# Kernel optimization log

Hardware: AMD Instinct MI355X
Metric: run time of the kernel (lower is better)

The kernel has to match this reference:

```python
import jax, jax.numpy as jnp
import numpy as np

N_NODES = 100000
N_EDGES = 1600000
IN_DIM = 256
OUT_DIM = 128


def setup_inputs() -> dict:
    key = jax.random.key(0)
    k1, k2, k3, k4 = jax.random.split(key, 4)
    x = jax.random.normal(k1, (N_NODES, IN_DIM), dtype=jnp.float32)
    edge_list = jax.random.randint(k2, (2, N_EDGES), 0, N_NODES, dtype=jnp.int64)
    # xavier_uniform with gain=1.414
    gW = 1.414 * np.sqrt(6.0 / (IN_DIM + OUT_DIM))
    W = jax.random.uniform(k3, (IN_DIM, OUT_DIM), dtype=jnp.float32, minval=-gW, maxval=gW)
    ga = 1.414 * np.sqrt(6.0 / (2 * OUT_DIM + 1))
    a = jax.random.uniform(k4, (2 * OUT_DIM, 1), dtype=jnp.float32, minval=-ga, maxval=ga)
    return {"x": x, "edge_list": edge_list, "W": W, "a": a}


def reference(x, edge_list, W, a):
    N = x.shape[0]
    src, dst = edge_list[0], edge_list[1]
    h = x @ W  # [N, out_dim]
    # cat([h[src], h[dst]]) @ a  ==  h[src] @ a[:d] + h[dst] @ a[d:]
    d = h.shape[1]
    s_src = (h @ a[:d]).ravel()  # [N]
    s_dst = (h @ a[d:]).ravel()  # [N]
    e = jax.nn.leaky_relu(s_src[src] + s_dst[dst], negative_slope=0.2)  # [E]
    # sparse softmax over rows (segments = src node)
    seg_max = jax.ops.segment_max(e, src, num_segments=N)  # [N]
    ex = jnp.exp(e - seg_max[src])  # [E]
    denom = jax.ops.segment_sum(ex, src, num_segments=N)  # [N]
    attn = ex / jnp.where(denom > 0, denom, 1.0)[src]  # [E]
    # sparse aggregate: h_prime[i] = sum_{edges (i,j)} attn_ij * h[j]
    h_prime = jax.ops.segment_sum(attn[:, None] * h[dst], src, num_segments=N)  # [N, d]
    return jax.nn.elu(h_prime)
```

## Files before the change

### kernel.cpp

```cpp
#include <hip/hip_runtime.h>
#include <hip/hip_bf16.h>
#include <cstdint>
#include <cstddef>

#define NN 100000
#define NE 1600000
#define KD 256
#define OD 128
#define NB 391
#define CAP 8192
#define NGB 782

typedef __attribute__((ext_vector_type(8))) __bf16 bf16x8;
typedef __attribute__((ext_vector_type(4))) float f32x4;
typedef __attribute__((ext_vector_type(8))) unsigned short ushort8;

static __device__ __forceinline__ unsigned short f2bf(float f) {
  return __builtin_bit_cast(unsigned short, (__bf16)f);
}
static __device__ __forceinline__ float bflo(unsigned p) {
  return __builtin_bit_cast(float, p << 16);
}
static __device__ __forceinline__ float bfhi(unsigned p) {
  return __builtin_bit_cast(float, p & 0xffff0000u);
}

__global__ void prep_wt_k(const float* __restrict__ W, unsigned short* __restrict__ Wt,
                          int* __restrict__ bcur) {
  const int i = blockIdx.x * 256 + threadIdx.x;
  const int k = i >> 7;
  const int n = i & 127;
  Wt[n * KD + k] = f2bf(W[i]);
  if (i < NB) bcur[i] = i * CAP;
}

__global__ __launch_bounds__(512, 4) void fused_k(
    const float* __restrict__ x, const unsigned short* __restrict__ Wt,
    const float* __restrict__ a, unsigned short* __restrict__ h,
    float* __restrict__ ssrc, float* __restrict__ sdst,
    const int* __restrict__ el, int* __restrict__ bcur,
    unsigned* __restrict__ stage) {
  __shared__ alignas(16) char smem[65536];
  const int t = threadIdx.x;

  if (blockIdx.x < NGB) {
    unsigned short* Bl = (unsigned short*)smem;
#pragma unroll
    for (int it = 0; it < 8; ++it) {
      const int c = it * 512 + t;
      const int r = c >> 5;
      const int c16 = c & 31;
      const ushort8 v = *(const ushort8*)(Wt + r * 256 + c16 * 8);
      const int byt = (r * 512 + c16 * 16) ^ ((r & 7) << 4);
      *(ushort8*)((char*)Bl + byt) = v;
    }
    const int lane = t & 63;
    const int wave = t >> 6;
    const int col = lane & 15;
    const int kg = lane >> 4;
    const int m0 = blockIdx.x * 128 + wave * 16;
    const int arow = m0 + col;
    const bool rowok = arow < NN;
    const float* __restrict__ xrow = x + (size_t)arow * KD;
    __syncthreads();

    f32x4 acc[8];
#pragma unroll
    for (int i = 0; i < 8; ++i) acc[i] = (f32x4)0.0f;

#pragma unroll
    for (int s = 0; s < 8; ++s) {
      const int kk = s * 32 + kg * 8;
      bf16x8 af = (bf16x8)(__bf16)0.0f;
      if (rowok) {
        const float4 f0 = *(const float4*)(xrow + kk);
        const float4 f1 = *(const float4*)(xrow + kk + 4);
        af[0] = (__bf16)f0.x; af[1] = (__bf16)f0.y; af[2] = (__bf16)f0.z; af[3] = (__bf16)f0.w;
        af[4] = (__bf16)f1.x; af[5] = (__bf16)f1.y; af[6] = (__bf16)f1.z; af[7] = (__bf16)f1.w;
      }
#pragma unroll
      for (int nt = 0; nt < 8; ++nt) {
        const int n = nt * 16 + col;
        const int byt = (n * 512 + s * 64 + kg * 16) ^ ((col & 7) << 4);
        const ushort8 bu = *(const ushort8*)((const char*)Bl + byt);
        const bf16x8 bf = __builtin_bit_cast(bf16x8, bu);
        acc[nt] = __builtin_amdgcn_mfma_f32_16x16x32_bf16(af, bf, acc[nt], 0, 0, 0);
      }
    }

    float ps[4] = {0.f, 0.f, 0.f, 0.f};
    float pd[4] = {0.f, 0.f, 0.f, 0.f};
#pragma unroll
    for (int nt = 0; nt < 8; ++nt) {
      const int n = nt * 16 + col;
      const float av = a[n];
      const float av2 = a[OD + n];
#pragma unroll
      for (int r = 0; r < 4; ++r) {
        const float v = acc[nt][r];
        const int row = m0 + kg * 4 + r;
        if (row < NN) h[(size_t)row * OD + n] = f2bf(v);
        ps[r] += v * av;
        pd[r] += v * av2;
      }
    }
#pragma unroll
    for (int off = 1; off < 16; off <<= 1) {
#pragma unroll
      for (int r = 0; r < 4; ++r) {
        ps[r] += __shfl_xor(ps[r], off, 64);
        pd[r] += __shfl_xor(pd[r], off, 64);
      }
    }
    if (col == 0) {
#pragma unroll
      for (int r = 0; r < 4; ++r) {
        const int row = m0 + kg * 4 + r;
        if (row < NN) {
          ssrc[row] = ps[r] * 1.442695041f;
          sdst[row] = pd[r] * 1.442695041f;
        }
      }
    }
  } else {
    unsigned* sorted = (unsigned*)smem;
    unsigned short* bkid = (unsigned short*)(smem + 16384);
    int* hist  = (int*)(smem + 24576);
    int* off   = (int*)(smem + 26144);
    int* cur   = (int*)(smem + 27712);
    int* delta = (int*)(smem + 29276);
    const int te = (blockIdx.x - NGB) * 4096 + t * 8;
    int s[8], d[8];
    bool valid[8];
#pragma unroll
    for (int u = 0; u < 8; ++u) valid[u] = (te + u) < NE;
    if (te + 7 < NE) {
      const int4 a0 = *(const int4*)(el + te);
      const int4 a1 = *(const int4*)(el + te + 4);
      const int4 b0 = *(const int4*)(el + NE + te);
      const int4 b1 = *(const int4*)(el + NE + te + 4);
      s[0] = a0.x; s[1] = a0.y; s[2] = a0.z; s[3] = a0.w;
      s[4] = a1.x; s[5] = a1.y; s[6] = a1.z; s[7] = a1.w;
      d[0] = b0.x; d[1] = b0.y; d[2] = b0.z; d[3] = b0.w;
      d[4] = b1.x; d[5] = b1.y; d[6] = b1.z; d[7] = b1.w;
    } else {
#pragma unroll
      for (int u = 0; u < 8; ++u) {
        s[u] = valid[u] ? el[te + u] : 0;
        d[u] = valid[u] ? el[NE + te + u] : 0;
      }
    }
    for (int i = t; i <= NB; i += 512) hist[i] = 0;
    __syncthreads();
#pragma unroll
    for (int u = 0; u < 8; ++u)
      if (valid[u]) atomicAdd(&hist[s[u] >> 8], 1);
    __syncthreads();
    if (t < 64) {
      int v[7];
      int sum = 0;
#pragma unroll
      for (int i = 0; i < 7; ++i) {
        const int idx = t * 7 + i;
        v[i] = (idx <= NB) ? hist[idx] : 0;
        sum += v[i];
      }
      int pre = sum;
#pragma unroll
      for (int o = 1; o < 64; o <<= 1) {
        const int nb = __shfl_up(pre, o, 64);
        if (t >= o) pre += nb;
      }
      pre -= sum;
      int run = pre;
#pragma unroll
      for (int i = 0; i < 7; ++i) {
        const int idx = t * 7 + i;
        if (idx <= NB) off[idx] = run;
        run += v[i];
      }
    }
    __syncthreads();
    for (int i = t; i < NB; i += 512) cur[i] = off[i];
    __syncthreads();
#pragma unroll
    for (int u = 0; u < 8; ++u)
      if (valid[u]) {
        const int b = s[u] >> 8;
        const int p = atomicAdd(&cur[b], 1);
        sorted[p] = ((unsigned)(s[u] & 255) << 17) | (unsigned)d[u];
        bkid[p] = (unsigned short)b;
      }
    __syncthreads();
    for (int b = t; b < NB; b += 512) {
      const int len = off[b + 1] - off[b];
      if (len > 0) {
        const int gb = atomicAdd(&bcur[b], len);
        delta[b] = gb - off[b];
      }
    }
    __syncthreads();
    const int n = off[NB];
    for (int i = t; i < n; i += 512) {
      const int b = bkid[i];
      const int pos = delta[b] + i;
      if (pos < (b + 1) * CAP) stage[pos] = sorted[i];
    }
  }
}

__global__ __launch_bounds__(512) void bscan_k(const int* __restrict__ bcur,
                                               int* __restrict__ bbase) {
  __shared__ int tmp[512];
  const int t = threadIdx.x;
  int v = 0;
  if (t < NB) {
    v = bcur[t] - t * CAP;
    v = v > CAP ? CAP : v;
  }
  tmp[t] = v;
  __syncthreads();
  for (int o = 1; o < 512; o <<= 1) {
    const int add = (t >= o) ? tmp[t - o] : 0;
    __syncthreads();
    tmp[t] += add;
    __syncthreads();
  }
  if (t < NB) bbase[t] = tmp[t] - v;
}

__global__ __launch_bounds__(256) void place2_k(const unsigned* __restrict__ stage,
                                                const int* __restrict__ bcur,
                                                const int* __restrict__ bbase,
                                                int* __restrict__ csrd,
                                                int* __restrict__ cnt,
                                                int* __restrict__ rowstart) {
  __shared__ unsigned ebuf[CAP];
  __shared__ int hist2[256];
  __shared__ int exc[256];
  __shared__ int cur2[256];
  const int b = blockIdx.x;
  const int t = threadIdx.x;
  int tot = bcur[b] - b * CAP;
  tot = tot > CAP ? CAP : tot;
  const int base = bbase[b];
  hist2[t] = 0;
  for (int i = t; i < tot; i += 256) ebuf[i] = stage[(size_t)b * CAP + i];
  __syncthreads();
  for (int i = t; i < tot; i += 256) atomicAdd(&hist2[ebuf[i] >> 17], 1);
  __syncthreads();
  if (t < 64) {
    int v[4];
    int sum = 0;
#pragma unroll
    for (int i = 0; i < 4; ++i) { v[i] = hist2[t * 4 + i]; sum += v[i]; }
    int pre = sum;
#pragma unroll
    for (int o = 1; o < 64; o <<= 1) {
      const int nb = __shfl_up(pre, o, 64);
      if (t >= o) pre += nb;
    }
    pre -= sum;
    int run = pre;
#pragma unroll
    for (int i = 0; i < 4; ++i) { exc[t * 4 + i] = run; run += v[i]; }
  }
  __syncthreads();
  const int node = b * 256 + t;
  if (node < NN) {
    cnt[node] = hist2[t];
    rowstart[node] = base + exc[t];
  }
  cur2[t] = exc[t];
  __syncthreads();
  for (int i = t; i < tot; i += 256) {
    const unsigned u = ebuf[i];
    const int p = atomicAdd(&cur2[u >> 17], 1);
    csrd[base + p] = (int)(u & 0x1ffffu);
  }
}

__global__ __launch_bounds__(256) void aggr_k(
    const unsigned short* __restrict__ h, const int* __restrict__ csrd,
    const int* __restrict__ rowstart, const int* __restrict__ cnt,
    const float* __restrict__ ssrc, const float* __restrict__ sdst,
    float* __restrict__ out) {
  const int lane = threadIdx.x & 63;
  const int node = blockIdx.x * 4 + (threadIdx.x >> 6);
  const int r0 = rowstart[node];
  const int deg = cnt[node];
  const int jend = r0 + deg;
  const float sbase = ssrc[node];
  const unsigned* __restrict__ hp = (const unsigned*)h;
  float a0 = 0.f, a1 = 0.f, sw = 0.f;
  const int nit = (deg + 7) >> 3;
  for (int it = 0; it < nit; ++it) {
    const int jb = r0 + it * 8;
    int d[8];
    unsigned pk[8];
    float w[8];
#pragma unroll
    for (int s = 0; s < 8; ++s) {
      const int jc = jb + s;
      const int jj = jc < jend ? jc : jend - 1;
      d[s] = csrd[jj];
    }
#pragma unroll
    for (int s = 0; s < 8; ++s)
      pk[s] = hp[(unsigned)d[s] * 64u + (unsigned)lane];
#pragma unroll
    for (int s = 0; s < 8; ++s) {
      const float sv = sbase + sdst[d[s]];
      float ww = exp2f(fmaxf(sv, 0.2f * sv));
      w[s] = (jb + s) < jend ? ww : 0.f;
      sw += w[s];
    }
#pragma unroll
    for (int s = 0; s < 8; ++s) {
      a0 = fmaf(w[s], bflo(pk[s]), a0);
      a1 = fmaf(w[s], bfhi(pk[s]), a1);
    }
  }
  const float inv = deg > 0 ? 1.0f / sw : 0.f;
  float o0 = a0 * inv, o1 = a1 * inv;
  o0 = o0 > 0.f ? o0 : __expf(o0) - 1.f;
  o1 = o1 > 0.f ? o1 : __expf(o1) - 1.f;
  *(float2*)(out + (size_t)node * OD + lane * 2) = make_float2(o0, o1);
}

extern "C" void kernel_launch(void* const* d_in, const int* in_sizes, int n_in,
                              void* d_out, int out_size, void* d_ws, size_t ws_size,
                              hipStream_t stream) {
  const float* x = (const float*)d_in[0];
  const int* el = (const int*)d_in[1];
  const float* W = (const float*)d_in[2];
  const float* a = (const float*)d_in[3];
  float* out = (float*)d_out;
  char* ws = (char*)d_ws;

  const size_t S = 400384;
  float* ssrc    = (float*)(ws + 0 * S);
  float* sdst    = (float*)(ws + 1 * S);
  int* cnt       = (int*)(ws + 2 * S);
  int* rowstart  = (int*)(ws + 3 * S);
  int* bcur      = (int*)(ws + 4 * S);
  int* bbase     = (int*)(ws + 4 * S + 2048);
  unsigned short* Wt = (unsigned short*)(ws + 4 * S + 8192);
  unsigned short* h  = (unsigned short*)(ws + 4 * S + 8192 + 65536);
  int* csrd = (int*)(ws + 4 * S + 8192 + 65536 + (size_t)NN * OD * 2);
  unsigned* stage = (unsigned*)d_out;

  prep_wt_k<<<128, 256, 0, stream>>>(W, Wt, bcur);
  fused_k<<<NGB + NB, 512, 0, stream>>>(x, Wt, a, h, ssrc, sdst, el, bcur, stage);
  bscan_k<<<1, 512, 0, stream>>>(bcur, bbase);
  place2_k<<<NB, 256, 0, stream>>>(stage, bcur, bbase, csrd, cnt, rowstart);
  aggr_k<<<NN / 4, 256, 0, stream>>>(h, csrd, rowstart, cnt, ssrc, sdst, out);
}
```

Baseline: 137.4 us.

## Precompute bf16 edge weights in CSR build and vectorize aggregation with 16-byte loads

The unnormalized attention weight exp2(leaky(ssrc+sdst)) is now computed once per edge during CSR placement, rounded to bf16 and packed into the upper 15 bits of each CSR entry alongside the 17-bit destination index. This removes the per-edge sdst gather and exp from the aggregation kernel. Aggregation is restructured so each wavefront handles 4 edges at once: 16 lanes per edge each load a 16-byte chunk of the bf16 h row, followed by a cross-group shuffle reduction and float4 stores. The sign bit of the weight is dropped and its precision is reduced, which holds because the weights are positive, and the reduction adds shuffle overhead.

```diff
diff --git a/kernel.cpp b/kernel.cpp
--- a/kernel.cpp
+++ b/kernel.cpp
@@ -232,10 +232,13 @@
 __global__ __launch_bounds__(256) void place2_k(const unsigned* __restrict__ stage,
                                                 const int* __restrict__ bcur,
                                                 const int* __restrict__ bbase,
-                                                int* __restrict__ csrd,
+                                                const float* __restrict__ ssrc,
+                                                const float* __restrict__ sdst,
+                                                unsigned* __restrict__ csrw,
                                                 int* __restrict__ cnt,
                                                 int* __restrict__ rowstart) {
   __shared__ unsigned ebuf[CAP];
+  __shared__ float sl[256];
   __shared__ int hist2[256];
   __shared__ int exc[256];
   __shared__ int cur2[256];
@@ -244,7 +247,9 @@
   int tot = bcur[b] - b * CAP;
   tot = tot > CAP ? CAP : tot;
   const int base = bbase[b];
+  const int node = b * 256 + t;
   hist2[t] = 0;
+  sl[t] = (node < NN) ? ssrc[node] : 0.f;
   for (int i = t; i < tot; i += 256) ebuf[i] = stage[(size_t)b * CAP + i];
   __syncthreads();
   for (int i = t; i < tot; i += 256) atomicAdd(&hist2[ebuf[i] >> 17], 1);
@@ -266,7 +271,6 @@
     for (int i = 0; i < 4; ++i) { exc[t * 4 + i] = run; run += v[i]; }
   }
   __syncthreads();
-  const int node = b * 256 + t;
   if (node < NN) {
     cnt[node] = hist2[t];
     rowstart[node] = base + exc[t];
@@ -275,57 +279,71 @@
   __syncthreads();
   for (int i = t; i < tot; i += 256) {
     const unsigned u = ebuf[i];
-    const int p = atomicAdd(&cur2[u >> 17], 1);
-    csrd[base + p] = (int)(u & 0x1ffffu);
+    const int s = u >> 17;
+    const unsigned d = u & 0x1ffffu;
+    const float sv = sl[s] + sdst[d];
+    const float w = exp2f(fmaxf(sv, 0.2f * sv));
+    unsigned wb = __builtin_bit_cast(unsigned, w);
+    wb += 0x7fffu + ((wb >> 16) & 1u);
+    const unsigned ent = ((wb >> 16) << 17) | d;
+    const int p = atomicAdd(&cur2[s], 1);
+    csrw[base + p] = ent;
   }
 }
 
 __global__ __launch_bounds__(256) void aggr_k(
-    const unsigned short* __restrict__ h, const int* __restrict__ csrd,
+    const unsigned short* __restrict__ h, const unsigned* __restrict__ csrw,
     const int* __restrict__ rowstart, const int* __restrict__ cnt,
-    const float* __restrict__ ssrc, const float* __restrict__ sdst,
     float* __restrict__ out) {
   const int lane = threadIdx.x & 63;
+  const int g = lane >> 4;
+  const int sub = lane & 15;
   const int node = blockIdx.x * 4 + (threadIdx.x >> 6);
   const int r0 = rowstart[node];
   const int deg = cnt[node];
   const int jend = r0 + deg;
-  const float sbase = ssrc[node];
-  const unsigned* __restrict__ hp = (const unsigned*)h;
-  float a0 = 0.f, a1 = 0.f, sw = 0.f;
+  const uint4* __restrict__ hp = (const uint4*)h;
+  float acc[8] = {0.f, 0.f, 0.f, 0.f, 0.f, 0.f, 0.f, 0.f};
+  float sw = 0.f;
   const int nit = (deg + 7) >> 3;
   for (int it = 0; it < nit; ++it) {
-    const int jb = r0 + it * 8;
-    int d[8];
-    unsigned pk[8];
-    float w[8];
-#pragma unroll
-    for (int s = 0; s < 8; ++s) {
-      const int jc = jb + s;
-      const int jj = jc < jend ? jc : jend - 1;
-      d[s] = csrd[jj];
-    }
-#pragma unroll
-    for (int s = 0; s < 8; ++s)
-      pk[s] = hp[(unsigned)d[s] * 64u + (unsigned)lane];
-#pragma unroll
-    for (int s = 0; s < 8; ++s) {
-      const float sv = sbase + sdst[d[s]];
-      float ww = exp2f(fmaxf(sv, 0.2f * sv));
-      w[s] = (jb + s) < jend ? ww : 0.f;
-      sw += w[s];
-    }
-#pragma unroll
-    for (int s = 0; s < 8; ++s) {
-      a0 = fmaf(w[s], bflo(pk[s]), a0);
-      a1 = fmaf(w[s], bfhi(pk[s]), a1);
-    }
+    const int j0 = r0 + it * 8 + g;
+    const int j1 = j0 + 4;
+    const unsigned u0 = csrw[j0 < jend ? j0 : r0];
+    const unsigned u1 = csrw[j1 < jend ? j1 : r0];
+    const unsigned d0 = u0 & 0x1ffffu;
+    const unsigned d1 = u1 & 0x1ffffu;
+    const uint4 p0 = hp[d0 * 16u + sub];
+    const uint4 p1 = hp[d1 * 16u + sub];
+    const float w0 = (j0 < jend) ? __builtin_bit_cast(float, (u0 >> 17) << 16) : 0.f;
+    const float w1 = (j1 < jend) ? __builtin_bit_cast(float, (u1 >> 17) << 16) : 0.f;
+    sw += w0 + w1;
+    const unsigned k0[4] = {p0.x, p0.y, p0.z, p0.w};
+    const unsigned k1[4] = {p1.x, p1.y, p1.z, p1.w};
+#pragma unroll
+    for (int q = 0; q < 4; ++q) {
+      acc[q * 2]     = fmaf(w0, bflo(k0[q]), fmaf(w1, bflo(k1[q]), acc[q * 2]));
+      acc[q * 2 + 1] = fmaf(w0, bfhi(k0[q]), fmaf(w1, bfhi(k1[q]), acc[q * 2 + 1]));
+    }
+  }
+#pragma unroll
+  for (int off = 16; off < 64; off <<= 1) {
+    sw += __shfl_xor(sw, off, 64);
+#pragma unroll
+    for (int q = 0; q < 8; ++q) acc[q] += __shfl_xor(acc[q], off, 64);
   }
   const float inv = deg > 0 ? 1.0f / sw : 0.f;
-  float o0 = a0 * inv, o1 = a1 * inv;
-  o0 = o0 > 0.f ? o0 : __expf(o0) - 1.f;
-  o1 = o1 > 0.f ? o1 : __expf(o1) - 1.f;
-  *(float2*)(out + (size_t)node * OD + lane * 2) = make_float2(o0, o1);
+  float o[8];
+#pragma unroll
+  for (int q = 0; q < 8; ++q) {
+    const float v = acc[q] * inv;
+    o[q] = v > 0.f ? v : __expf(v) - 1.f;
+  }
+  if (lane < 16) {
+    float4* op = (float4*)(out + (size_t)node * OD + sub * 8);
+    op[0] = make_float4(o[0], o[1], o[2], o[3]);
+    op[1] = make_float4(o[4], o[5], o[6], o[7]);
+  }
 }
 
 extern "C" void kernel_launch(void* const* d_in, const int* in_sizes, int n_in,
@@ -347,12 +365,12 @@
   int* bbase     = (int*)(ws + 4 * S + 2048);
   unsigned short* Wt = (unsigned short*)(ws + 4 * S + 8192);
   unsigned short* h  = (unsigned short*)(ws + 4 * S + 8192 + 65536);
-  int* csrd = (int*)(ws + 4 * S + 8192 + 65536 + (size_t)NN * OD * 2);
+  unsigned* csrw = (unsigned*)(ws + 4 * S + 8192 + 65536 + (size_t)NN * OD * 2);
   unsigned* stage = (unsigned*)d_out;
 
   prep_wt_k<<<128, 256, 0, stream>>>(W, Wt, bcur);
   fused_k<<<NGB + NB, 512, 0, stream>>>(x, Wt, a, h, ssrc, sdst, el, bcur, stage);
   bscan_k<<<1, 512, 0, stream>>>(bcur, bbase);
-  place2_k<<<NB, 256, 0, stream>>>(stage, bcur, bbase, csrd, cnt, rowstart);
-  aggr_k<<<NN / 4, 256, 0, stream>>>(h, csrd, rowstart, cnt, ssrc, sdst, out);
-}
+  place2_k<<<NB, 256, 0, stream>>>(stage, bcur, bbase, ssrc, sdst, csrw, cnt, rowstart);
+  aggr_k<<<NN / 4, 256, 0, stream>>>(h, csrw, rowstart, cnt, out);
+}
```

After: 122.1 us. 11.1% less time.
